# Performance work log

Hardware: AMD Instinct MI355X
Metric: run time of the kernel (lower is better)

## Reference

```python
import jax, jax.numpy as jnp
import numpy as np

D_MODEL = 768
NHEAD = 12
HEAD_DIM = D_MODEL // NHEAD
B, L = 8, 1024


def setup_inputs() -> dict:
    key = jax.random.key(0)
    ks = jax.random.split(key, 10)
    s = 0.02  # init scale for weights
    return {
        "x": jax.random.normal(ks[0], (B, L, D_MODEL), dtype=jnp.float32),
        "pos": jax.random.normal(ks[1], (B, L, D_MODEL), dtype=jnp.float32),
        "qkv_w": jax.random.normal(ks[2], (3 * D_MODEL, D_MODEL), dtype=jnp.float32) * s,
        "qkv_b": jnp.zeros((3 * D_MODEL,), dtype=jnp.float32),
        "pq_w": jax.random.normal(ks[3], (D_MODEL, D_MODEL), dtype=jnp.float32) * s,
        "pq_b": jnp.zeros((D_MODEL,), dtype=jnp.float32),
        "pk_w": jax.random.normal(ks[4], (D_MODEL, D_MODEL), dtype=jnp.float32) * s,
        "pk_b": jnp.zeros((D_MODEL,), dtype=jnp.float32),
    }


def reference(x, pos, qkv_w, qkv_b, pq_w, pq_b, pk_w, pk_b):
    b, l, d = x.shape
    h, hd = NHEAD, HEAD_DIM

    qkv = x @ qkv_w.T + qkv_b  # (b, l, 3d)
    q, k, v = jnp.split(qkv, 3, axis=-1)
    # rearrange 'b l (h d) -> b l h d'
    q = q.reshape(b, l, h, hd)
    k = k.reshape(b, l, h, hd)
    v = v.reshape(b, l, h, hd)

    pq = (pos @ pq_w.T + pq_b).reshape(b, l, h, hd)
    pk = (pos @ pk_w.T + pk_b).reshape(b, l, h, hd)

    CC = jnp.einsum('bnhd,blhd->bhnl', q, k)
    CP = jnp.einsum('bnhd,blhd->bhnl', q, pq)
    PC = jnp.einsum('bnhd,blhd->bhnl', k, pk)

    # Faithful to source: only PC is scaled (operator precedence in original)
    scale = (3 * d) ** 0.5
    attn = jax.nn.softmax(CC + CP + PC / scale, axis=-1)

    out = jnp.einsum('bhnl,blhd->bnhd', attn, v)  # (b, n, h, hd)
    return out
```

## Files before the change

### kernel.cpp

```cpp
#include <hip/hip_runtime.h>
#include <hip/hip_bf16.h>

#define NHEAD 12
#define BATCH 8
#define SEQ 1024
#define LOG2E 1.4426950408889634f

typedef __bf16 bf16x8 __attribute__((ext_vector_type(8)));
typedef float  f32x4  __attribute__((ext_vector_type(4)));

#define WAITVM0 asm volatile("s_waitcnt vmcnt(0)" ::: "memory")
#define WAITVM4 asm volatile("s_waitcnt vmcnt(4)" ::: "memory")
#define WAITVM1 asm volatile("s_waitcnt vmcnt(1)" ::: "memory")

#define MFMA(A, B, C) __builtin_amdgcn_mfma_f32_16x16x32_bf16(A, B, C, 0, 0, 0)

__device__ __forceinline__ unsigned short f2bf(float f) {
    union { float f; unsigned u; } v; v.f = f;
    unsigned u = v.u;
    u += 0x7fff + ((u >> 16) & 1);
    return (unsigned short)(u >> 16);
}

__device__ __forceinline__ unsigned pkbf(float a, float b) {
    union { __hip_bfloat162 h; unsigned u; } cv;
    cv.h = __float22bfloat162_rn(make_float2(a, b));
    return cv.u;
}

__device__ __forceinline__ void gload_lds16(const void* g, void* l) {
    __builtin_amdgcn_global_load_lds(
        (const __attribute__((address_space(1))) unsigned*)g,
        (__attribute__((address_space(3))) unsigned*)l, 16, 0, 0);
}

#define SZ_X    6291456
#define SZ_QKVW 1769472
#define SZ_PW   589824
#define CONV_TOTAL 15532032

__global__ __launch_bounds__(256) void convert_kernel(
    const float* __restrict__ x, const float* __restrict__ pos,
    const float* __restrict__ qkv_w, const float* __restrict__ pq_w,
    const float* __restrict__ pk_w, unsigned short* __restrict__ dst)
{
    const size_t i4 = ((size_t)blockIdx.x * 256 + threadIdx.x) * 4;
    if (i4 >= CONV_TOTAL) return;
    const float* src; size_t off;
    if (i4 < SZ_X)                { src = x;     off = i4; }
    else if (i4 < 2 * SZ_X)       { src = pos;   off = i4 - SZ_X; }
    else if (i4 < 2 * SZ_X + SZ_QKVW) { src = qkv_w; off = i4 - 2 * SZ_X; }
    else if (i4 < 2 * SZ_X + SZ_QKVW + SZ_PW) { src = pq_w; off = i4 - 2 * SZ_X - SZ_QKVW; }
    else                          { src = pk_w;  off = i4 - 2 * SZ_X - SZ_QKVW - SZ_PW; }
    float4 v = *(const float4*)(src + off);
    ushort4 o;
    o.x = f2bf(v.x); o.y = f2bf(v.y); o.z = f2bf(v.z); o.w = f2bf(v.w);
    *(ushort4*)(dst + i4) = o;
}


#define PROJ_STAGE(K0, AS, BS) do {                                          \
    const int k0_ = (K0);                                                    \
    const unsigned short* asrc_; int acol_;                                  \
    if (g == 4)                    { asrc_ = posb; acol_ = k0_; }            \
    else if (g == 3 && k0_ >= 768) { asrc_ = posb; acol_ = k0_ - 768; }      \
    else                           { asrc_ = xb;   acol_ = k0_; }            \
    gload_lds16(asrc_ + (size_t)(m0 + r0) * 768 + acol_ + q0 * 8, &AS[base0]);\
    gload_lds16(asrc_ + (size_t)(m0 + r1) * 768 + acol_ + q1 * 8, &AS[base1]);\
    const unsigned short* wsrc_; int wro_, wco_;                             \
    if (g <= 2)       { wsrc_ = qkvw; wro_ = n0;        wco_ = k0_; }        \
    else if (g == 3) {                                                       \
        if (k0_ < 768) { wsrc_ = qkvw; wro_ = n0 - 1536; wco_ = k0_; }       \
        else           { wsrc_ = pqw;  wro_ = n0 - 2304; wco_ = k0_ - 768; } \
    } else            { wsrc_ = pkw;  wro_ = n0 - 3072; wco_ = k0_; }        \
    gload_lds16(wsrc_ + (size_t)(wro_ + r0) * 768 + wco_ + q0 * 8, &BS[base0]);\
    gload_lds16(wsrc_ + (size_t)(wro_ + r1) * 768 + wco_ + q1 * 8, &BS[base1]);\
} while (0)

#define PROJ_COMPUTE(AS, BS) do {                                            \
    bf16x8 af[4], bfr[4];                                                    \
    _Pragma("unroll")                                                        \
    for (int mt = 0; mt < 4; ++mt) {                                         \
        const int rr = wm + mt * 16 + col16;                                 \
        af[mt] = *(const bf16x8*)&AS[rr * 32 + ((quad ^ ((rr >> 1) & 3)) * 8)];\
    }                                                                        \
    _Pragma("unroll")                                                        \
    for (int nt = 0; nt < 4; ++nt) {                                         \
        const int rr = wn + nt * 16 + col16;                                 \
        bfr[nt] = *(const bf16x8*)&BS[rr * 32 + ((quad ^ ((rr >> 1) & 3)) * 8)];\
    }                                                                        \
    _Pragma("unroll")                                                        \
    for (int mt = 0; mt < 4; ++mt)                                           \
        _Pragma("unroll")                                                    \
        for (int nt = 0; nt < 4; ++nt)                                       \
            acc[mt][nt] = MFMA(af[mt], bfr[nt], acc[mt][nt]);                \
} while (0)

__global__ __launch_bounds__(256, 3) void proj_kernel(
    const unsigned short* __restrict__ xb, const unsigned short* __restrict__ posb,
    const unsigned short* __restrict__ qkvw, const unsigned short* __restrict__ pqw,
    const unsigned short* __restrict__ pkw,
    const float* __restrict__ qkv_b, const float* __restrict__ pq_b,
    const float* __restrict__ pk_b,
    unsigned short* __restrict__ Q2, unsigned short* __restrict__ K2,
    unsigned short* __restrict__ Vt, int band)
{
    __shared__ unsigned short As0[128 * 32];
    __shared__ unsigned short As1[128 * 32];
    __shared__ unsigned short As2[128 * 32];
    __shared__ unsigned short Bs0[128 * 32];
    __shared__ unsigned short Bs1[128 * 32];
    __shared__ unsigned short Bs2[128 * 32];

    const int id  = blockIdx.x;
    const int xcd = id & 7;
    const int idx = id >> 3;
    const int nt30 = (idx / band + 18) % 30;
    const int m0 = (xcd * band + idx % band) * 128;
    const int n0 = nt30 * 128;
    const int g  = n0 / 768;
    const int nk = (g == 3) ? 48 : 24;

    const int tid   = threadIdx.x;
    const int lane  = tid & 63;
    const int w     = tid >> 6;
    const int wm    = (w & 1) * 64;
    const int wn    = (w >> 1) * 64;
    const int quad  = lane >> 4;
    const int col16 = lane & 15;

    const int c0 = w * 64 + lane;
    const int c1 = c0 + 256;
    const int r0 = c0 >> 2, q0 = (c0 & 3) ^ ((c0 >> 3) & 3);
    const int r1 = c1 >> 2, q1 = (c1 & 3) ^ ((c1 >> 3) & 3);
    const int base0 = (w * 64) * 8;
    const int base1 = (w * 64 + 256) * 8;

    f32x4 acc[4][4];
    const f32x4 fzero = {0.f, 0.f, 0.f, 0.f};
#pragma unroll
    for (int mt = 0; mt < 4; ++mt)
#pragma unroll
        for (int nt = 0; nt < 4; ++nt) acc[mt][nt] = fzero;

    PROJ_STAGE(0, As0, Bs0);
    PROJ_STAGE(32, As1, Bs1);

    for (int kt = 0; kt < nk; kt += 3) {
        WAITVM4;
        __syncthreads();
        PROJ_STAGE((kt + 2) * 32, As2, Bs2);
        PROJ_COMPUTE(As0, Bs0);

        WAITVM4;
        __syncthreads();
        if (kt + 3 < nk) PROJ_STAGE((kt + 3) * 32, As0, Bs0);
        PROJ_COMPUTE(As1, Bs1);

        if (kt + 3 >= nk) { WAITVM0; } else { WAITVM4; }
        __syncthreads();
        if (kt + 4 < nk) PROJ_STAGE((kt + 4) * 32, As1, Bs1);
        PROJ_COMPUTE(As2, Bs2);
    }

    if (g == 2) {
#pragma unroll
        for (int mt = 0; mt < 4; ++mt) {
            const int mbase = m0 + wm + mt * 16 + quad * 4;
#pragma unroll
            for (int nt = 0; nt < 4; ++nt) {
                const int n = n0 + wn + nt * 16 + col16;
                const int b = mbase >> 10, l0 = mbase & 1023;
                const int c = n - 1536, h = c >> 6, dd = c & 63;
                const float bias = qkv_b[n];
                uint2 pk;
                pk.x = pkbf(acc[mt][nt][0] + bias, acc[mt][nt][1] + bias);
                pk.y = pkbf(acc[mt][nt][2] + bias, acc[mt][nt][3] + bias);
                *(uint2*)&Vt[((size_t)(b * NHEAD + h) * 64 + dd) * 1024 + l0] = pk;
            }
        }
    } else {
#pragma unroll
        for (int p = 0; p < 4; ++p) {
            __syncthreads();
            if ((wm >> 6) == (p >> 1)) {
#pragma unroll
                for (int mth = 0; mth < 2; ++mth) {
                    const int mt = ((p & 1) << 1) | mth;
#pragma unroll
                    for (int nt = 0; nt < 4; ++nt) {
                        const int n = n0 + wn + nt * 16 + col16;
                        float badd, bmul;
                        if (g == 0)      { badd = qkv_b[n];                         bmul = LOG2E; }
                        else if (g == 1) { badd = qkv_b[n];                         bmul = LOG2E / 48.0f; }
                        else if (g == 3) { badd = qkv_b[n - 1536] + pq_b[n - 2304]; bmul = 1.0f; }
                        else             { badd = pk_b[n - 3072];                   bmul = 1.0f; }
                        const int lrb  = mth * 16 + quad * 4;
                        const int ccol = wn + nt * 16 + col16;
#pragma unroll
                        for (int r = 0; r < 4; ++r)
                            As0[(lrb + r) * 128 + ccol] =
                                f2bf((acc[mt][nt][r] + badd) * bmul);
                    }
                }
            }
            __syncthreads();
#pragma unroll
            for (int j = 0; j < 2; ++j) {
                const int u = tid + 256 * j;
                const int rowp = u >> 4;
                const int seg  = u & 15;
                const int m = m0 + p * 32 + rowp;
                const int b = m >> 10, l = m & 1023;
                const int n = n0 + seg * 8;
                uint4 v = *(const uint4*)&As0[rowp * 128 + seg * 8];
                unsigned short* dst;
                if (g == 0)      { const int h = n >> 6, dd = n & 63;
                                   dst = &Q2[((size_t)(b * NHEAD + h) * 1024 + l) * 128 + dd]; }
                else if (g == 1) { const int c = n - 768,  h = c >> 6, dd = c & 63;
                                   dst = &Q2[((size_t)(b * NHEAD + h) * 1024 + l) * 128 + 64 + dd]; }
                else if (g == 3) { const int c = n - 2304, h = c >> 6, dd = c & 63;
                                   dst = &K2[((size_t)(b * NHEAD + h) * 1024 + l) * 128 + dd]; }
                else             { const int c = n - 3072, h = c >> 6, dd = c & 63;
                                   dst = &K2[((size_t)(b * NHEAD + h) * 1024 + l) * 128 + 64 + dd]; }
                *(uint4*)dst = v;
            }
        }
    }
}


#define ATTN_STG(J0, KS, VS) do {                                            \
    const int j0_ = (J0);                                                    \
    gload_lds16(&K2[q2base + (size_t)(j0_ + kr0) * 128 + kc0 * 8], &KS[kbase0]);\
    gload_lds16(&K2[q2base + (size_t)(j0_ + kr1) * 128 + kc1 * 8], &KS[kbase1]);\
    gload_lds16(&Vt[vtbase + (size_t)vr * 1024 + j0_ + vc * 8],    &VS[vbase]);\
} while (0)

#define ATTN_PV(VS, PSR) do {                                                \
    bf16x8 bp0 = *(const bf16x8*)&PSR[w][col16][quad * 8];                   \
    bf16x8 bp1 = *(const bf16x8*)&PSR[w][16 + col16][quad * 8];              \
    _Pragma("unroll")                                                        \
    for (int c2 = 0; c2 < 4; ++c2) {                                         \
        const int rv = c2 * 16 + col16;                                      \
        bf16x8 av = *(const bf16x8*)&VS[rv * 32 + ((quad ^ ((rv >> 2) & 3)) * 8)];\
        o[0][c2] = MFMA(av, bp0, o[0][c2]);                                  \
        o[1][c2] = MFMA(av, bp1, o[1][c2]);                                  \
    }                                                                        \
} while (0)

#define ATTN_QK(KS, PSW) do {                                                \
    f32x4 st[2][2] = {{fzero, fzero}, {fzero, fzero}};                       \
    _Pragma("unroll")                                                        \
    for (int kk = 0; kk < 4; ++kk) {                                         \
        const int rrj0 = col16, rrj1 = 16 + col16;                           \
        bf16x8 kf0 = *(const bf16x8*)&KS[rrj0 * 128 + (((kk * 4 + quad) ^ (rrj0 & 15)) * 8)];\
        bf16x8 kf1 = *(const bf16x8*)&KS[rrj1 * 128 + (((kk * 4 + quad) ^ (rrj1 & 15)) * 8)];\
        _Pragma("unroll")                                                    \
        for (int qt = 0; qt < 2; ++qt) {                                     \
            st[0][qt] = MFMA(kf0, bq[qt][kk], st[0][qt]);                    \
            st[1][qt] = MFMA(kf1, bq[qt][kk], st[1][qt]);                    \
        }                                                                    \
    }                                                                        \
    _Pragma("unroll")                                                        \
    for (int qt = 0; qt < 2; ++qt) {                                         \
        float p0[4], p1[4], s = 0.f;                                         \
        _Pragma("unroll")                                                    \
        for (int r = 0; r < 4; ++r) {                                        \
            p0[r] = __builtin_amdgcn_exp2f(st[0][qt][r]);                    \
            p1[r] = __builtin_amdgcn_exp2f(st[1][qt][r]);                    \
            s += p0[r] + p1[r];                                              \
        }                                                                    \
        lsum[qt] += s;                                                       \
        uint2 w0, w1;                                                        \
        w0.x = pkbf(p0[0], p0[1]); w0.y = pkbf(p0[2], p0[3]);                \
        w1.x = pkbf(p1[0], p1[1]); w1.y = pkbf(p1[2], p1[3]);                \
        *(uint2*)&PSW[w][qt * 16 + col16][quad * 4]      = w0;               \
        *(uint2*)&PSW[w][qt * 16 + col16][16 + quad * 4] = w1;               \
    }                                                                        \
} while (0)

#define ATTN_PHASE(J, KQK, KST, VPV, VST, PSW, PSR, DOPV, DOST) do {         \
    WAITVM1;                                                                 \
    __syncthreads();                                                         \
    if (DOST) ATTN_STG(((J) + 1) * 32, KST, VST);                            \
    if (DOPV) ATTN_PV(VPV, PSR);                                             \
    ATTN_QK(KQK, PSW);                                                       \
} while (0)

__global__ __launch_bounds__(256, 3) void attn_kernel(
    const unsigned short* __restrict__ Q2, const unsigned short* __restrict__ K2,
    const unsigned short* __restrict__ Vt, float* __restrict__ out, int b0)
{
    __shared__ unsigned short K2sA[32 * 128];
    __shared__ unsigned short K2sB[32 * 128];
    __shared__ unsigned short VtX[64 * 32];
    __shared__ unsigned short VtY[64 * 32];
    __shared__ unsigned short VtZ[64 * 32];
    __shared__ unsigned short Ps0[4][32][40];
    __shared__ unsigned short Ps1[4][32][40];

    const int bh_l = blockIdx.x;
    const int b = b0 + bh_l / NHEAD, h = bh_l % NHEAD;
    const int tid   = threadIdx.x;
    const int lane  = tid & 63;
    const int w     = tid >> 6;
    const int quad  = lane >> 4;
    const int col16 = lane & 15;
    const int qbase = blockIdx.y * 128 + w * 32;

    const size_t q2base = (size_t)bh_l * 1024 * 128;
    const size_t vtbase = (size_t)bh_l * 64 * 1024;

    const int kL0 = w * 64 + lane, kL1 = kL0 + 256;
    const int kr0 = kL0 >> 4, kc0 = (kL0 & 15) ^ (kr0 & 15);
    const int kr1 = kL1 >> 4, kc1 = (kL1 & 15) ^ (kr1 & 15);
    const int vL  = w * 64 + lane;
    const int vr  = vL >> 2,  vc  = (vL & 3) ^ ((vL >> 4) & 3);
    const int kbase0 = (w * 64) * 8, kbase1 = (w * 64 + 256) * 8;
    const int vbase  = (w * 64) * 8;

    bf16x8 bq[2][4];
#pragma unroll
    for (int qt = 0; qt < 2; ++qt)
#pragma unroll
        for (int kk = 0; kk < 4; ++kk)
            bq[qt][kk] = *(const bf16x8*)&Q2[q2base +
                (size_t)(qbase + qt * 16 + col16) * 128 + kk * 32 + quad * 8];

    f32x4 o[2][4];
    const f32x4 fzero = {0.f, 0.f, 0.f, 0.f};
#pragma unroll
    for (int qt = 0; qt < 2; ++qt)
#pragma unroll
        for (int c2 = 0; c2 < 4; ++c2) o[qt][c2] = fzero;
    float lsum[2] = {0.f, 0.f};

    ATTN_STG(0, K2sA, VtX);

    ATTN_PHASE(0, K2sA, K2sB, VtZ, VtY, Ps0, Ps1, 0, 1);

    for (int j = 1; j < 31; j += 6) {
        ATTN_PHASE(j + 0, K2sB, K2sA, VtX, VtZ, Ps1, Ps0, 1, 1);
        ATTN_PHASE(j + 1, K2sA, K2sB, VtY, VtX, Ps0, Ps1, 1, 1);
        ATTN_PHASE(j + 2, K2sB, K2sA, VtZ, VtY, Ps1, Ps0, 1, 1);
        ATTN_PHASE(j + 3, K2sA, K2sB, VtX, VtZ, Ps0, Ps1, 1, 1);
        ATTN_PHASE(j + 4, K2sB, K2sA, VtY, VtX, Ps1, Ps0, 1, 1);
        ATTN_PHASE(j + 5, K2sA, K2sB, VtZ, VtY, Ps0, Ps1, 1, 1);
    }

    ATTN_PHASE(31, K2sB, K2sA, VtX, VtZ, Ps1, Ps0, 1, 0);

    WAITVM0;
    __syncthreads();
    ATTN_PV(VtY, Ps1);

#pragma unroll
    for (int qt = 0; qt < 2; ++qt) {
        lsum[qt] += __shfl_xor(lsum[qt], 16, 64);
        lsum[qt] += __shfl_xor(lsum[qt], 32, 64);
    }

#pragma unroll
    for (int qt = 0; qt < 2; ++qt) {
        const float inv = 1.0f / lsum[qt];
        const int q = qbase + qt * 16 + col16;
#pragma unroll
        for (int c2 = 0; c2 < 4; ++c2) {
#pragma unroll
            for (int r = 0; r < 4; ++r) {
                const int dd = c2 * 16 + quad * 4 + r;
                out[(((size_t)(b * 1024 + q)) * 12 + h) * 64 + dd] = o[qt][c2][r] * inv;
            }
        }
    }
}

extern "C" void kernel_launch(void* const* d_in, const int* in_sizes, int n_in,
                              void* d_out, int out_size, void* d_ws, size_t ws_size,
                              hipStream_t stream) {
    const float* x     = (const float*)d_in[0];
    const float* pos   = (const float*)d_in[1];
    const float* qkv_w = (const float*)d_in[2];
    const float* qkv_b = (const float*)d_in[3];
    const float* pq_w  = (const float*)d_in[4];
    const float* pq_b  = (const float*)d_in[5];
    const float* pk_w  = (const float*)d_in[6];
    const float* pk_b  = (const float*)d_in[7];
    float* out = (float*)d_out;

    unsigned short* ws   = (unsigned short*)d_ws;
    unsigned short* xb   = ws;
    unsigned short* posb = xb + SZ_X;
    unsigned short* qkvw = posb + SZ_X;
    unsigned short* pqw  = qkvw + SZ_QKVW;
    unsigned short* pkw  = pqw + SZ_PW;
    unsigned short* cbuf = pkw + SZ_PW;

    const size_t conv_bytes = (size_t)CONV_TOTAL * 2;
    const size_t per_batch  = (size_t)NHEAD * 1024 * 128 * 4
                            + (size_t)NHEAD * 64 * 1024 * 2;
    int cb = BATCH;
    while (cb > 1 && conv_bytes + (size_t)cb * per_batch > ws_size) cb >>= 1;

    unsigned short* Q2 = cbuf;
    unsigned short* K2 = Q2 + (size_t)cb * NHEAD * 1024 * 128;
    unsigned short* Vt = K2 + (size_t)cb * NHEAD * 1024 * 128;

    convert_kernel<<<(CONV_TOTAL / 4 + 255) / 256, 256, 0, stream>>>(
        x, pos, qkv_w, pq_w, pk_w, ws);

    for (int b0 = 0; b0 < BATCH; b0 += cb) {
        proj_kernel<<<dim3(cb * 240), 256, 0, stream>>>(
            xb + (size_t)b0 * 1024 * 768, posb + (size_t)b0 * 1024 * 768,
            qkvw, pqw, pkw, qkv_b, pq_b, pk_b, Q2, K2, Vt, cb);
        attn_kernel<<<dim3(cb * NHEAD, 8), 256, 0, stream>>>(Q2, K2, Vt, out, b0);
    }
}
```

Measured before the change: 234.7 us.

## Reuse K projection partial sums to eliminate duplicate K GEMM tile group

```diff
diff --git a/kernel.cpp b/kernel.cpp
--- a/kernel.cpp
+++ b/kernel.cpp
@@ -62,17 +62,18 @@
 #define PROJ_STAGE(K0, AS, BS) do {                                          \
     const int k0_ = (K0);                                                    \
     const unsigned short* asrc_; int acol_;                                  \
-    if (g == 4)                    { asrc_ = posb; acol_ = k0_; }            \
-    else if (g == 3 && k0_ >= 768) { asrc_ = posb; acol_ = k0_ - 768; }      \
-    else                           { asrc_ = xb;   acol_ = k0_; }            \
+    if (gg == 3)                    { asrc_ = posb; acol_ = k0_; }           \
+    else if (gg == 2 && k0_ >= 768) { asrc_ = posb; acol_ = k0_ - 768; }     \
+    else                            { asrc_ = xb;   acol_ = k0_; }           \
     gload_lds16(asrc_ + (size_t)(m0 + r0) * 768 + acol_ + q0 * 8, &AS[base0]);\
     gload_lds16(asrc_ + (size_t)(m0 + r1) * 768 + acol_ + q1 * 8, &AS[base1]);\
     const unsigned short* wsrc_; int wro_, wco_;                             \
-    if (g <= 2)       { wsrc_ = qkvw; wro_ = n0;        wco_ = k0_; }        \
-    else if (g == 3) {                                                       \
-        if (k0_ < 768) { wsrc_ = qkvw; wro_ = n0 - 1536; wco_ = k0_; }       \
-        else           { wsrc_ = pqw;  wro_ = n0 - 2304; wco_ = k0_ - 768; } \
-    } else            { wsrc_ = pkw;  wro_ = n0 - 3072; wco_ = k0_; }        \
+    if (gg == 0)      { wsrc_ = qkvw; wro_ = colbase;        wco_ = k0_; }   \
+    else if (gg == 1) { wsrc_ = qkvw; wro_ = 1536 + colbase; wco_ = k0_; }   \
+    else if (gg == 2) {                                                      \
+        if (k0_ < 768) { wsrc_ = qkvw; wro_ = 768 + colbase; wco_ = k0_; }   \
+        else           { wsrc_ = pqw;  wro_ = colbase;       wco_ = k0_ - 768; }\
+    } else            { wsrc_ = pkw;  wro_ = colbase;        wco_ = k0_; }   \
     gload_lds16(wsrc_ + (size_t)(wro_ + r0) * 768 + wco_ + q0 * 8, &BS[base0]);\
     gload_lds16(wsrc_ + (size_t)(wro_ + r1) * 768 + wco_ + q1 * 8, &BS[base1]);\
 } while (0)
@@ -94,6 +95,43 @@
         _Pragma("unroll")                                                    \
         for (int nt = 0; nt < 4; ++nt)                                       \
             acc[mt][nt] = MFMA(af[mt], bfr[nt], acc[mt][nt]);                \
+} while (0)
+
+#define PROJ_EPI(SRC, BADDEXPR, BMULV, DSTEXPR) do {                         \
+    _Pragma("unroll")                                                        \
+    for (int p = 0; p < 4; ++p) {                                            \
+        __syncthreads();                                                     \
+        if ((wm >> 6) == (p >> 1)) {                                         \
+            _Pragma("unroll")                                                \
+            for (int mth = 0; mth < 2; ++mth) {                              \
+                const int mt = ((p & 1) << 1) | mth;                         \
+                _Pragma("unroll")                                            \
+                for (int nt = 0; nt < 4; ++nt) {                             \
+                    const int c = colbase + wn + nt * 16 + col16;            \
+                    const float badd = (BADDEXPR);                           \
+                    const int lrb  = mth * 16 + quad * 4;                    \
+                    const int ccol = wn + nt * 16 + col16;                   \
+                    _Pragma("unroll")                                        \
+                    for (int r = 0; r < 4; ++r)                              \
+                        As0[(lrb + r) * 128 + ccol] =                        \
+                            f2bf((SRC[mt][nt][r] + badd) * (BMULV));         \
+                }                                                            \
+            }                                                                \
+        }                                                                    \
+        __syncthreads();                                                     \
+        _Pragma("unroll")                                                    \
+        for (int j = 0; j < 2; ++j) {                                        \
+            const int u = tid + 256 * j;                                     \
+            const int rowp = u >> 4;                              \
+            const int seg  = u & 15;                      \
+            const int m = m0 + p * 32 + rowp;                                \
+            const int b = m >> 10, l = m & 1023;                             \
+            const int c = colbase + seg * 8;                                 \
+            const int h = c >> 6, dd = c & 63;                               \
+            uint4 v = *(const uint4*)&As0[rowp * 128 + seg * 8];             \
+            *(uint4*)(DSTEXPR) = v;                                          \
+        }                                                                    \
+    }                                                                        \
 } while (0)
 
 __global__ __launch_bounds__(256, 3) void proj_kernel(
@@ -115,11 +153,11 @@
     const int id  = blockIdx.x;
     const int xcd = id & 7;
     const int idx = id >> 3;
-    const int nt30 = (idx / band + 18) % 30;
+    const int t24 = (idx / band + 12) % 24;
     const int m0 = (xcd * band + idx % band) * 128;
-    const int n0 = nt30 * 128;
-    const int g  = n0 / 768;
-    const int nk = (g == 3) ? 48 : 24;
+    const int gg = t24 / 6;
+    const int colbase = (t24 % 6) * 128;
+    const int nk = (gg == 2) ? 48 : 24;
 
     const int tid   = threadIdx.x;
     const int lane  = tid & 63;
@@ -161,71 +199,53 @@
         __syncthreads();
         if (kt + 4 < nk) PROJ_STAGE((kt + 4) * 32, As1, Bs1);
         PROJ_COMPUTE(As2, Bs2);
-    }
-
-    if (g == 2) {
+
+        if (gg == 2 && kt == 21) {
+#pragma unroll
+            for (int mt = 0; mt < 4; ++mt) {
+                const int mbase = m0 + wm + mt * 16 + quad * 4;
+#pragma unroll
+                for (int nt = 0; nt < 4; ++nt) {
+                    const int c = colbase + wn + nt * 16 + col16;
+                    const float bias = qkv_b[768 + c];
+                    const int h = c >> 6, dd = c & 63;
+#pragma unroll
+                    for (int r = 0; r < 4; ++r) {
+                        const int m = mbase + r;
+                        const int b = m >> 10, l = m & 1023;
+                        Q2[((size_t)(b * NHEAD + h) * 1024 + l) * 128 + 64 + dd] =
+                            f2bf((acc[mt][nt][r] + bias) * (LOG2E / 48.0f));
+                    }
+                }
+            }
+        }
+    }
+
+    if (gg == 1) {
 #pragma unroll
         for (int mt = 0; mt < 4; ++mt) {
             const int mbase = m0 + wm + mt * 16 + quad * 4;
 #pragma unroll
             for (int nt = 0; nt < 4; ++nt) {
-                const int n = n0 + wn + nt * 16 + col16;
+                const int c = colbase + wn + nt * 16 + col16;
                 const int b = mbase >> 10, l0 = mbase & 1023;
-                const int c = n - 1536, h = c >> 6, dd = c & 63;
-                const float bias = qkv_b[n];
+                const int h = c >> 6, dd = c & 63;
+                const float bias = qkv_b[1536 + c];
                 uint2 pk;
                 pk.x = pkbf(acc[mt][nt][0] + bias, acc[mt][nt][1] + bias);
                 pk.y = pkbf(acc[mt][nt][2] + bias, acc[mt][nt][3] + bias);
                 *(uint2*)&Vt[((size_t)(b * NHEAD + h) * 64 + dd) * 1024 + l0] = pk;
             }
         }
+    } else if (gg == 0) {
+        PROJ_EPI(acc, qkv_b[c], LOG2E,
+                 &Q2[((size_t)(b * NHEAD + h) * 1024 + l) * 128 + dd]);
+    } else if (gg == 2) {
+        PROJ_EPI(acc, qkv_b[768 + c] + pq_b[c], 1.0f,
+                 &K2[((size_t)(b * NHEAD + h) * 1024 + l) * 128 + dd]);
     } else {
-#pragma unroll
-        for (int p = 0; p < 4; ++p) {
-            __syncthreads();
-            if ((wm >> 6) == (p >> 1)) {
-#pragma unroll
-                for (int mth = 0; mth < 2; ++mth) {
-                    const int mt = ((p & 1) << 1) | mth;
-#pragma unroll
-                    for (int nt = 0; nt < 4; ++nt) {
-                        const int n = n0 + wn + nt * 16 + col16;
-                        float badd, bmul;
-                        if (g == 0)      { badd = qkv_b[n];                         bmul = LOG2E; }
-                        else if (g == 1) { badd = qkv_b[n];                         bmul = LOG2E / 48.0f; }
-                        else if (g == 3) { badd = qkv_b[n - 1536] + pq_b[n - 2304]; bmul = 1.0f; }
-                        else             { badd = pk_b[n - 3072];                   bmul = 1.0f; }
-                        const int lrb  = mth * 16 + quad * 4;
-                        const int ccol = wn + nt * 16 + col16;
-#pragma unroll
-                        for (int r = 0; r < 4; ++r)
-                            As0[(lrb + r) * 128 + ccol] =
-                                f2bf((acc[mt][nt][r] + badd) * bmul);
-                    }
-                }
-            }
-            __syncthreads();
-#pragma unroll
-            for (int j = 0; j < 2; ++j) {
-                const int u = tid + 256 * j;
-                const int rowp = u >> 4;
-                const int seg  = u & 15;
-                const int m = m0 + p * 32 + rowp;
-                const int b = m >> 10, l = m & 1023;
-                const int n = n0 + seg * 8;
-                uint4 v = *(const uint4*)&As0[rowp * 128 + seg * 8];
-                unsigned short* dst;
-                if (g == 0)      { const int h = n >> 6, dd = n & 63;
-                                   dst = &Q2[((size_t)(b * NHEAD + h) * 1024 + l) * 128 + dd]; }
-                else if (g == 1) { const int c = n - 768,  h = c >> 6, dd = c & 63;
-                                   dst = &Q2[((size_t)(b * NHEAD + h) * 1024 + l) * 128 + 64 + dd]; }
-                else if (g == 3) { const int c = n - 2304, h = c >> 6, dd = c & 63;
-                                   dst = &K2[((size_t)(b * NHEAD + h) * 1024 + l) * 128 + dd]; }
-                else             { const int c = n - 3072, h = c >> 6, dd = c & 63;
-                                   dst = &K2[((size_t)(b * NHEAD + h) * 1024 + l) * 128 + 64 + dd]; }
-                *(uint4*)dst = v;
-            }
-        }
+        PROJ_EPI(acc, pk_b[c], 1.0f,
+                 &K2[((size_t)(b * NHEAD + h) * 1024 + l) * 128 + 64 + dd]);
     }
 }
 
@@ -411,7 +431,7 @@
         x, pos, qkv_w, pq_w, pk_w, ws);
 
     for (int b0 = 0; b0 < BATCH; b0 += cb) {
-        proj_kernel<<<dim3(cb * 240), 256, 0, stream>>>(
+        proj_kernel<<<dim3(cb * 192), 256, 0, stream>>>(
             xb + (size_t)b0 * 1024 * 768, posb + (size_t)b0 * 1024 * 768,
             qkvw, pqw, pkw, qkv_b, pq_b, pk_b, Q2, K2, Vt, cb);
         attn_kernel<<<dim3(cb * NHEAD, 8), 256, 0, stream>>>(Q2, K2, Vt, out, b0);
```

New measurement: 251.9 us. 1.07x slower.
